# Kernel tuning notes

Hardware: AMD Instinct MI355X
Metric: run time of the kernel (lower is better)

The kernel has to match this reference:

```python
import jax, jax.numpy as jnp
import numpy as np

PROMPT_LEN = 2048
VOCAB = 49408
DIM = 768


def setup_inputs() -> dict:
    key = jax.random.key(0)
    k1, k2 = jax.random.split(key)
    # prompt_embs initialized ~ N(0, 0.02) per nn.init.normal_(std=0.02)
    prompt_embs = jax.random.normal(k1, (PROMPT_LEN, DIM), dtype=jnp.float32) * 0.02
    # codebook (CLIP embedding table), fixed data (not a trainable param)
    clip_embs = jax.random.normal(k2, (VOCAB, DIM), dtype=jnp.float32)
    return {"prompt_embs": prompt_embs, "clip_embs": clip_embs}


def _find_nearest(prompt_embs, clip_embs):
    # torch.cdist with p=2 -> Euclidean distance. argmin is invariant under sqrt,
    # so we use the expanded squared-distance form (single GEMM + norms),
    # avoiding materializing the [P, D]-broadcast difference tensor.
    p_sq = jnp.sum(prompt_embs * prompt_embs, axis=-1, keepdims=True)  # [P, 1]
    c_sq = jnp.sum(clip_embs * clip_embs, axis=-1)                      # [V]
    cross = jnp.einsum("pd,vd->pv", prompt_embs, clip_embs)            # [P, V]
    d2 = p_sq + c_sq[None, :] - 2.0 * cross                             # [P, V]
    return jnp.argmin(d2, axis=1)                                       # [P]


def reference(prompt_embs, clip_embs):
    prompt_ids = _find_nearest(prompt_embs, clip_embs)      # [P] int
    vocab_embs = clip_embs[prompt_ids, :]                   # [P, D] gather
    # straight-through: value = vocab_embs, gradient flows to prompt_embs
    out_embs = jax.lax.stop_gradient(vocab_embs - prompt_embs) + prompt_embs
    return out_embs, prompt_ids
```

## Files before the change

### kernel.cpp

```cpp
#include <hip/hip_runtime.h>
#include <float.h>

#define PROMPT_LEN 2048
#define VOCAB 49408
#define DIM 768
#define ROWS_TOTAL (VOCAB + PROMPT_LEN)
#define NS 8
#define NMI (PROMPT_LEN / 64)
#define BM 64
#define BN 64
#define KCH 128
#define NCHUNK (DIM / KCH)
#define LDK (KCH + 8)
#define CAND_MAX 4096
#define EPS 0.008f

typedef __attribute__((ext_vector_type(8))) short s8v;
typedef __attribute__((ext_vector_type(4))) float fx4;


__device__ inline unsigned short f2bf(float x) {
    unsigned u = __float_as_uint(x);
    u += 0x7FFFu + ((u >> 16) & 1u);
    return (unsigned short)(u >> 16);
}

__device__ inline void merge2(float& b1, float& b2, int& bi,
                              float y1, float y2, int yi) {
    if (y1 < b1) { b2 = fminf(b1, y2); b1 = y1; bi = yi; }
    else         { b2 = fminf(b2, fminf(y1, y2)); }
}

__device__ inline void conv_row(const float* __restrict__ src,
                                unsigned short* __restrict__ dH,
                                unsigned short* __restrict__ dL, int lane) {
    #pragma unroll
    for (int i = 0; i < 3; ++i) {
        float4 x = ((const float4*)src)[i * 64 + lane];
        ushort4 h, l;
        h.x = f2bf(x.x); l.x = f2bf(x.x - __uint_as_float((unsigned)h.x << 16));
        h.y = f2bf(x.y); l.y = f2bf(x.y - __uint_as_float((unsigned)h.y << 16));
        h.z = f2bf(x.z); l.z = f2bf(x.z - __uint_as_float((unsigned)h.z << 16));
        h.w = f2bf(x.w); l.w = f2bf(x.w - __uint_as_float((unsigned)h.w << 16));
        ((ushort4*)dH)[i * 64 + lane] = h;
        ((ushort4*)dL)[i * 64 + lane] = l;
    }
}

__global__ void __launch_bounds__(256) k_sumsq(const float* __restrict__ prompt,
                                               const float* __restrict__ clip,
                                               float* __restrict__ csq,
                                               unsigned* __restrict__ scal) {
    int tid  = threadIdx.x;
    int wid  = tid >> 6;
    int lane = tid & 63;
    int base = blockIdx.x * 32 + wid * 8;

    if (blockIdx.x == 0 && tid == 0) scal[0] = 0u;

    float locMin = FLT_MAX, locMax = 0.f;
    for (int r = base; r < base + 8; r += 2) {
        const float* s0 = (r     < VOCAB) ? clip + (size_t)r * DIM
                                          : prompt + (size_t)(r - VOCAB) * DIM;
        const float* s1 = (r + 1 < VOCAB) ? clip + (size_t)(r + 1) * DIM
                                          : prompt + (size_t)(r + 1 - VOCAB) * DIM;
        float4 a0 = ((const float4*)s0)[lane];
        float4 a1 = ((const float4*)s0)[64 + lane];
        float4 a2 = ((const float4*)s0)[128 + lane];
        float4 b0 = ((const float4*)s1)[lane];
        float4 b1 = ((const float4*)s1)[64 + lane];
        float4 b2 = ((const float4*)s1)[128 + lane];
        float sA = a0.x*a0.x + a0.y*a0.y + a0.z*a0.z + a0.w*a0.w
                 + a1.x*a1.x + a1.y*a1.y + a1.z*a1.z + a1.w*a1.w
                 + a2.x*a2.x + a2.y*a2.y + a2.z*a2.z + a2.w*a2.w;
        float sB = b0.x*b0.x + b0.y*b0.y + b0.z*b0.z + b0.w*b0.w
                 + b1.x*b1.x + b1.y*b1.y + b1.z*b1.z + b1.w*b1.w
                 + b2.x*b2.x + b2.y*b2.y + b2.z*b2.z + b2.w*b2.w;
        #pragma unroll
        for (int m = 32; m >= 1; m >>= 1) {
            sA += __shfl_xor(sA, m, 64);
            sB += __shfl_xor(sB, m, 64);
        }
        if (r < VOCAB)     locMin = fminf(locMin, sA); else locMax = fmaxf(locMax, sA);
        if (r + 1 < VOCAB) locMin = fminf(locMin, sB); else locMax = fmaxf(locMax, sB);
        if (lane == 0) {
            if (r < VOCAB)     csq[r] = sA;
            if (r + 1 < VOCAB) csq[r + 1] = sB;
        }
    }
    __shared__ float smn[4], smx[4];
    if (lane == 0) { smn[wid] = locMin; smx[wid] = locMax; }
    __syncthreads();
    if (tid == 0) {
        float mn = FLT_MAX, mx = 0.f;
        #pragma unroll
        for (int w = 0; w < 4; ++w) { mn = fminf(mn, smn[w]); mx = fmaxf(mx, smx[w]); }
        atomicMin(&scal[1], __float_as_uint(mn));
        atomicMax((int*)&scal[2], (int)__float_as_uint(mx));
    }
}

__global__ void __launch_bounds__(256) k_compact_convert(
        const float* __restrict__ prompt, const float* __restrict__ clip,
        const float* __restrict__ csq,
        int* __restrict__ cand, float* __restrict__ candCsq,
        unsigned* __restrict__ scal, int* __restrict__ cnt,
        unsigned short* __restrict__ PbH, unsigned short* __restrict__ PbL,
        unsigned short* __restrict__ CbH, unsigned short* __restrict__ CbL) {
    float cmin    = __uint_as_float(scal[1]);
    float pmax_sq = __uint_as_float(scal[2]);
    float B  = sqrtf(pmax_sq) * 1.0001f + 1e-6f;
    float U  = cmin + 2.f * B * sqrtf(cmin) + 1.0f;
    float sT = B + sqrtf(B * B + U);
    float T  = sT * sT;

    int tid = threadIdx.x;
    int v   = blockIdx.x * 256 + tid;
    if (blockIdx.x == 0) {
        if (tid == 0) scal[3] = 0u;
        if (tid < NMI) cnt[tid] = 0;
    }
    __shared__ int cntS, basep;
    __shared__ int kvS[256];
    if (tid == 0) cntS = 0;
    __syncthreads();
    float cs = csq[v];
    int keep = (cs <= T);
    int pos = 0;
    if (keep) pos = atomicAdd(&cntS, 1);
    __syncthreads();
    if (tid == 0 && cntS > 0) basep = atomicAdd((int*)&scal[0], cntS);
    __syncthreads();
    if (keep) {
        cand[basep + pos]    = v;
        candCsq[basep + pos] = cs;
        kvS[pos] = v;
    }
    __syncthreads();

    int nk   = cntS;
    int wid  = tid >> 6;
    int lane = tid & 63;
    for (int i = wid; i < nk; i += 4) {
        int dst = basep + i;
        if (dst >= CAND_MAX) break;
        conv_row(clip + (size_t)kvS[i] * DIM,
                 CbH + (size_t)dst * DIM, CbL + (size_t)dst * DIM, lane);
    }
    #pragma unroll
    for (int j = wid; j < 11; j += 4) {
        int r = blockIdx.x + 193 * j;
        if (r < PROMPT_LEN)
            conv_row(prompt + (size_t)r * DIM,
                     PbH + (size_t)r * DIM, PbL + (size_t)r * DIM, lane);
    }
}

__global__ void __launch_bounds__(256, 2)
k_score(const unsigned short* __restrict__ PbH, const unsigned short* __restrict__ PbL,
        const unsigned short* __restrict__ CbH, const unsigned short* __restrict__ CbL,
        const float* __restrict__ candCsq, const int* __restrict__ cand,
        unsigned* __restrict__ scal, int* __restrict__ cnt,
        float* __restrict__ AB1, float* __restrict__ AB2, int* __restrict__ AIdx,
        const float* __restrict__ prompt, const float* __restrict__ clip,
        int* __restrict__ amb, float* __restrict__ out) {
    int mi = blockIdx.x & (NMI - 1);
    int s  = blockIdx.x >> 5;
    int m0 = mi * BM;
    int rawCount = (int)scal[0];
    int count = rawCount > CAND_MAX ? CAND_MAX : rawCount;
    int ntiles = (count + BN - 1) / BN;

    int tid  = threadIdx.x;
    int lane = tid & 63;
    int wid  = tid >> 6;
    int wr32 = (wid >> 1) * 32;
    int wc32 = (wid & 1) * 32;
    int l15  = lane & 15;
    int l4   = lane >> 4;

    __shared__ unsigned short Ah[BM][LDK], Al[BM][LDK];
    __shared__ unsigned short Bh[BN][LDK], Bl[BN][LDK];
    __shared__ int   candS[BN];
    __shared__ float csqS[BN];
    __shared__ float mB1[BM][4], mB2[BM][4];
    __shared__ int   mBI[BM][4];
    __shared__ int   winS[BM], clearS[BM];
    __shared__ int   lastS;

    int srow[4], scol[4], offA[4];
    #pragma unroll
    for (int f = 0; f < 4; ++f) {
        int j = tid + 256 * f;
        srow[f] = j >> 4;
        scol[f] = (j & 15) * 8;
        offA[f] = (m0 + srow[f]) * DIM + scol[f];
    }

    float rb1[2][4], rb2[2][4]; int rbi[2][4];
    #pragma unroll
    for (int fm = 0; fm < 2; ++fm)
        #pragma unroll
        for (int j = 0; j < 4; ++j) { rb1[fm][j] = FLT_MAX; rb2[fm][j] = FLT_MAX; rbi[fm][j] = 0x7fffffff; }

    for (int tile = s; tile < ntiles; tile += NS) {
        __syncthreads();
        if (tid < BN) {
            int ci = tile * BN + tid;
            candS[tid] = (ci < count) ? cand[ci] : 0;
            csqS[tid]  = (ci < count) ? candCsq[ci] : FLT_MAX;
        }

        int offB[4];
        #pragma unroll
        for (int f = 0; f < 4; ++f) {
            int rowc = tile * BN + srow[f];
            if (rowc >= count) rowc = 0;
            offB[f] = rowc * DIM + scol[f];
        }

        fx4 acc00 = {0.f,0.f,0.f,0.f}, acc01 = {0.f,0.f,0.f,0.f};
        fx4 acc10 = {0.f,0.f,0.f,0.f}, acc11 = {0.f,0.f,0.f,0.f};

        s8v rAh[4], rAl[4], rBh[4], rBl[4];
        #pragma unroll
        for (int f = 0; f < 4; ++f) {
            rAh[f] = *(const s8v*)(PbH + offA[f]);
            rAl[f] = *(const s8v*)(PbL + offA[f]);
            rBh[f] = *(const s8v*)(CbH + offB[f]);
            rBl[f] = *(const s8v*)(CbL + offB[f]);
        }

        #pragma unroll
        for (int kc = 0; kc < NCHUNK; ++kc) {
            __syncthreads();
            #pragma unroll
            for (int f = 0; f < 4; ++f) {
                *(s8v*)&Ah[srow[f]][scol[f]] = rAh[f];
                *(s8v*)&Al[srow[f]][scol[f]] = rAl[f];
                *(s8v*)&Bh[srow[f]][scol[f]] = rBh[f];
                *(s8v*)&Bl[srow[f]][scol[f]] = rBl[f];
            }
            __syncthreads();
            if (kc + 1 < NCHUNK) {
                int off = (kc + 1) * KCH;
                #pragma unroll
                for (int f = 0; f < 4; ++f) {
                    rAh[f] = *(const s8v*)(PbH + offA[f] + off);
                    rAl[f] = *(const s8v*)(PbL + offA[f] + off);
                    rBh[f] = *(const s8v*)(CbH + offB[f] + off);
                    rBl[f] = *(const s8v*)(CbL + offB[f] + off);
                }
            }
            #pragma unroll
            for (int kk = 0; kk < KCH / 32; ++kk) {
                int ko = kk * 32 + l4 * 8;
                s8v ah0 = *(const s8v*)&Ah[wr32      + l15][ko];
                s8v ah1 = *(const s8v*)&Ah[wr32 + 16 + l15][ko];
                s8v al0 = *(const s8v*)&Al[wr32      + l15][ko];
                s8v al1 = *(const s8v*)&Al[wr32 + 16 + l15][ko];
                s8v bh0 = *(const s8v*)&Bh[wc32      + l15][ko];
                s8v bh1 = *(const s8v*)&Bh[wc32 + 16 + l15][ko];
                s8v bl0 = *(const s8v*)&Bl[wc32      + l15][ko];
                s8v bl1 = *(const s8v*)&Bl[wc32 + 16 + l15][ko];
                acc00 = __builtin_amdgcn_mfma_f32_16x16x32_bf16(ah0, bh0, acc00, 0, 0, 0);
                acc01 = __builtin_amdgcn_mfma_f32_16x16x32_bf16(ah0, bh1, acc01, 0, 0, 0);
                acc10 = __builtin_amdgcn_mfma_f32_16x16x32_bf16(ah1, bh0, acc10, 0, 0, 0);
                acc11 = __builtin_amdgcn_mfma_f32_16x16x32_bf16(ah1, bh1, acc11, 0, 0, 0);
                acc00 = __builtin_amdgcn_mfma_f32_16x16x32_bf16(al0, bh0, acc00, 0, 0, 0);
                acc01 = __builtin_amdgcn_mfma_f32_16x16x32_bf16(al0, bh1, acc01, 0, 0, 0);
                acc10 = __builtin_amdgcn_mfma_f32_16x16x32_bf16(al1, bh0, acc10, 0, 0, 0);
                acc11 = __builtin_amdgcn_mfma_f32_16x16x32_bf16(al1, bh1, acc11, 0, 0, 0);
                acc00 = __builtin_amdgcn_mfma_f32_16x16x32_bf16(ah0, bl0, acc00, 0, 0, 0);
                acc01 = __builtin_amdgcn_mfma_f32_16x16x32_bf16(ah0, bl1, acc01, 0, 0, 0);
                acc10 = __builtin_amdgcn_mfma_f32_16x16x32_bf16(ah1, bl0, acc10, 0, 0, 0);
                acc11 = __builtin_amdgcn_mfma_f32_16x16x32_bf16(ah1, bl1, acc11, 0, 0, 0);
            }
        }

        float cs0 = csqS[wc32 + l15];       int v0 = candS[wc32 + l15];
        float cs1 = csqS[wc32 + 16 + l15];  int v1 = candS[wc32 + 16 + l15];
        #pragma unroll
        for (int j = 0; j < 4; ++j) {
            if (cs0 < FLT_MAX) {
                float d2 = fmaf(-2.f, acc00[j], cs0);
                if (d2 < rb1[0][j]) { rb2[0][j] = rb1[0][j]; rb1[0][j] = d2; rbi[0][j] = v0; }
                else if (d2 <= rb2[0][j]) rb2[0][j] = d2;
                d2 = fmaf(-2.f, acc10[j], cs0);
                if (d2 < rb1[1][j]) { rb2[1][j] = rb1[1][j]; rb1[1][j] = d2; rbi[1][j] = v0; }
                else if (d2 <= rb2[1][j]) rb2[1][j] = d2;
            }
            if (cs1 < FLT_MAX) {
                float d2 = fmaf(-2.f, acc01[j], cs1);
                if (d2 < rb1[0][j]) { rb2[0][j] = rb1[0][j]; rb1[0][j] = d2; rbi[0][j] = v1; }
                else if (d2 <= rb2[0][j]) rb2[0][j] = d2;
                d2 = fmaf(-2.f, acc11[j], cs1);
                if (d2 < rb1[1][j]) { rb2[1][j] = rb1[1][j]; rb1[1][j] = d2; rbi[1][j] = v1; }
                else if (d2 <= rb2[1][j]) rb2[1][j] = d2;
            }
        }
    }

    #pragma unroll
    for (int fm = 0; fm < 2; ++fm)
        #pragma unroll
        for (int j = 0; j < 4; ++j) {
            float b1 = rb1[fm][j], b2 = rb2[fm][j]; int bi = rbi[fm][j];
            #pragma unroll
            for (int msk = 1; msk <= 8; msk <<= 1) {
                float y1 = __shfl_xor(b1, msk, 64);
                float y2 = __shfl_xor(b2, msk, 64);
                int   yi = __shfl_xor(bi, msk, 64);
                merge2(b1, b2, bi, y1, y2, yi);
            }
            if (l15 == 0) {
                int rl = wr32 + fm * 16 + l4 * 4 + j;
                mB1[rl][wid & 1] = b1; mB2[rl][wid & 1] = b2; mBI[rl][wid & 1] = bi;
            }
        }
    __syncthreads();
    if (tid < BM) {
        float B1 = mB1[tid][0], B2 = mB2[tid][0]; int BI = mBI[tid][0];
        merge2(B1, B2, BI, mB1[tid][1], mB2[tid][1], mBI[tid][1]);
        int m = m0 + tid;
        __hip_atomic_store(&AB1[m * NS + s], B1, __ATOMIC_RELAXED, __HIP_MEMORY_SCOPE_AGENT);
        __hip_atomic_store(&AB2[m * NS + s], B2, __ATOMIC_RELAXED, __HIP_MEMORY_SCOPE_AGENT);
        __hip_atomic_store(&AIdx[m * NS + s], BI, __ATOMIC_RELAXED, __HIP_MEMORY_SCOPE_AGENT);
    }
    __syncthreads();
    if (tid == 0) {
        __threadfence();
        int old = atomicAdd(&cnt[mi], 1);
        lastS = (old == NS - 1);
    }
    __syncthreads();
    if (!lastS) return;
    __threadfence();

    {
        int r = tid & 63, g = tid >> 6;
        int m = m0 + r;
        float b1 = FLT_MAX, b2 = FLT_MAX; int bi = 0x7fffffff;
        #pragma unroll
        for (int ss = 0; ss < 2; ++ss) {
            int s2 = g * 2 + ss;
            float y1 = __hip_atomic_load(&AB1[m * NS + s2], __ATOMIC_RELAXED, __HIP_MEMORY_SCOPE_AGENT);
            float y2 = __hip_atomic_load(&AB2[m * NS + s2], __ATOMIC_RELAXED, __HIP_MEMORY_SCOPE_AGENT);
            int   yi = __hip_atomic_load(&AIdx[m * NS + s2], __ATOMIC_RELAXED, __HIP_MEMORY_SCOPE_AGENT);
            merge2(b1, b2, bi, y1, y2, yi);
        }
        mB1[r][g] = b1; mB2[r][g] = b2; mBI[r][g] = bi;
    }
    __syncthreads();
    if (tid < BM) {
        float B1 = mB1[tid][0], B2 = mB2[tid][0]; int BI = mBI[tid][0];
        #pragma unroll
        for (int gg = 1; gg < 4; ++gg)
            merge2(B1, B2, BI, mB1[tid][gg], mB2[tid][gg], mBI[tid][gg]);
        int clear = (rawCount <= CAND_MAX) && (B2 - B1 >= EPS);
        winS[tid] = BI; clearS[tid] = clear;
        if (!clear) {
            int pos = atomicAdd((int*)&scal[3], 1);
            amb[pos] = m0 + tid;
        }
    }
    __syncthreads();
    for (int rr = wid; rr < BM; rr += 4) {
        if (!clearS[rr]) continue;
        int mm = m0 + rr, win = winS[rr];
        const float* crow = clip + (size_t)win * DIM;
        const float* prow = prompt + (size_t)mm * DIM;
        #pragma unroll
        for (int i = 0; i < 3; ++i) {
            float4 c = ((const float4*)crow)[i * 64 + lane];
            float4 p = ((const float4*)prow)[i * 64 + lane];
            float4 o;
            o.x = (c.x - p.x) + p.x;
            o.y = (c.y - p.y) + p.y;
            o.z = (c.z - p.z) + p.z;
            o.w = (c.w - p.w) + p.w;
            ((float4*)(out + (size_t)mm * DIM))[i * 64 + lane] = o;
        }
        if (lane == 0) out[(size_t)PROMPT_LEN * DIM + mm] = (float)win;
    }
}

__global__ void __launch_bounds__(1024) k_fallback(const float* __restrict__ prompt,
                                                   const float* __restrict__ clip,
                                                   const int* __restrict__ cand,
                                                   const unsigned* __restrict__ scal,
                                                   const int* __restrict__ amb,
                                                   float* __restrict__ out) {
    int nAmb  = (int)scal[3];
    int count = (int)scal[0];
    int tid  = threadIdx.x;
    int wid  = tid >> 6;
    int lane = tid & 63;

    __shared__ double fB[16];
    __shared__ int    fI[16];
    __shared__ int    sWin;

    for (int a = blockIdx.x; a < nAmb; a += gridDim.x) {
        int m = amb[a];
        const float* prow = prompt + (size_t)m * DIM;
        double pd[12];
        #pragma unroll
        for (int i = 0; i < 3; ++i) {
            float4 v = ((const float4*)prow)[i * 64 + lane];
            pd[i*4+0] = (double)v.x; pd[i*4+1] = (double)v.y;
            pd[i*4+2] = (double)v.z; pd[i*4+3] = (double)v.w;
        }
        double best = 1e300;
        int bestIdx = 0x7fffffff;
        for (int ci = wid; ci < count; ci += 16) {
            int v = cand[ci];
            const float* crow = clip + (size_t)v * DIM;
            double sd = 0.0;
            #pragma unroll
            for (int i = 0; i < 3; ++i) {
                float4 c = ((const float4*)crow)[i * 64 + lane];
                double d0 = (double)c.x - pd[i*4+0];
                double d1 = (double)c.y - pd[i*4+1];
                double d2 = (double)c.z - pd[i*4+2];
                double d3 = (double)c.w - pd[i*4+3];
                sd = fma(d0, d0, sd); sd = fma(d1, d1, sd);
                sd = fma(d2, d2, sd); sd = fma(d3, d3, sd);
            }
            #pragma unroll
            for (int msk = 32; msk >= 1; msk >>= 1) sd += __shfl_xor(sd, msk, 64);
            if (sd < best || (sd == best && v < bestIdx)) { best = sd; bestIdx = v; }
        }
        if (lane == 0) { fB[wid] = best; fI[wid] = bestIdx; }
        __syncthreads();
        if (tid == 0) {
            double b = fB[0]; int bi2 = fI[0];
            #pragma unroll
            for (int w = 1; w < 16; ++w)
                if (fB[w] < b || (fB[w] == b && fI[w] < bi2)) { b = fB[w]; bi2 = fI[w]; }
            sWin = bi2;
        }
        __syncthreads();
        int win = sWin;

        if (tid < 192) {
            float4 c = ((const float4*)(clip + (size_t)win * DIM))[tid];
            float4 p = ((const float4*)prow)[tid];
            float4 o;
            o.x = (c.x - p.x) + p.x;
            o.y = (c.y - p.y) + p.y;
            o.z = (c.z - p.z) + p.z;
            o.w = (c.w - p.w) + p.w;
            ((float4*)(out + (size_t)m * DIM))[tid] = o;
        }
        if (tid == 0) out[(size_t)PROMPT_LEN * DIM + m] = (float)win;
        __syncthreads();
    }
}

extern "C" void kernel_launch(void* const* d_in, const int* in_sizes, int n_in,
                              void* d_out, int out_size, void* d_ws, size_t ws_size,
                              hipStream_t stream) {
    const float* prompt = (const float*)d_in[0];
    const float* clip   = (const float*)d_in[1];
    float* out = (float*)d_out;

    char* w = (char*)d_ws;
    float*    csq     = (float*)w;                 w += (size_t)VOCAB * 4;
    int*      cand    = (int*)w;                   w += (size_t)VOCAB * 4;
    float*    candCsq = (float*)w;                 w += (size_t)VOCAB * 4;
    unsigned* scal    = (unsigned*)w;              w += 32;
    float*    AB1     = (float*)w;                 w += (size_t)PROMPT_LEN * NS * 4;
    float*    AB2     = (float*)w;                 w += (size_t)PROMPT_LEN * NS * 4;
    int*      AIdx    = (int*)w;                   w += (size_t)PROMPT_LEN * NS * 4;
    int*      amb     = (int*)w;                   w += (size_t)PROMPT_LEN * 4;
    int*      cnt     = (int*)w;                   w += 128;
    unsigned short* PbH = (unsigned short*)w;      w += (size_t)PROMPT_LEN * DIM * 2;
    unsigned short* PbL = (unsigned short*)w;      w += (size_t)PROMPT_LEN * DIM * 2;
    unsigned short* CbH = (unsigned short*)w;      w += (size_t)CAND_MAX * DIM * 2;
    unsigned short* CbL = (unsigned short*)w;      w += (size_t)CAND_MAX * DIM * 2;

    k_sumsq<<<ROWS_TOTAL / 32, 256, 0, stream>>>(prompt, clip, csq, scal);
    k_compact_convert<<<VOCAB / 256, 256, 0, stream>>>(prompt, clip, csq, cand, candCsq,
                                                       scal, cnt, PbH, PbL, CbH, CbL);
    k_score<<<NMI * NS, 256, 0, stream>>>(PbH, PbL, CbH, CbL, candCsq, cand, scal, cnt,
                                          AB1, AB2, AIdx, prompt, clip, amb, out);
    k_fallback<<<128, 1024, 0, stream>>>(prompt, clip, cand, scal, amb, out);
}
```

Measured before the change: 332.8 us.

## Fuse four kernels into one cooperative persistent kernel with grid syncs

Replaces the four separate launches (sum of squares, compaction/conversion, scoring, fallback) with a single cooperative kernel of 256 blocks. Grid-wide barriers separate the stages. Prompt bf16 hi/lo splitting moves into the sum-of-squares pass so each prompt row is read only once. This removes launch gaps and inter-kernel drains. The costs are that only 256 blocks run the memory-bound stages, the fallback uses 4 waves per block instead of 16, and the grid-sync overhead is added.

```diff
diff --git a/kernel.cpp b/kernel.cpp
--- a/kernel.cpp
+++ b/kernel.cpp
@@ -1,12 +1,15 @@
 #include <hip/hip_runtime.h>
+#include <hip/hip_cooperative_groups.h>
 #include <float.h>
+
+namespace cg = cooperative_groups;
 
 #define PROMPT_LEN 2048
 #define VOCAB 49408
 #define DIM 768
 #define ROWS_TOTAL (VOCAB + PROMPT_LEN)
 #define NS 8
-#define NMI (PROMPT_LEN / 64)
+#define NMI 32
 #define BM 64
 #define BN 64
 #define KCH 128
@@ -25,10 +28,14 @@
     return (unsigned short)(u >> 16);
 }
 
-__device__ inline void merge2(float& b1, float& b2, int& bi,
-                              float y1, float y2, int yi) {
-    if (y1 < b1) { b2 = fminf(b1, y2); b1 = y1; bi = yi; }
-    else         { b2 = fminf(b2, fminf(y1, y2)); }
+__device__ inline void split_store(float4 x, unsigned short* dH, unsigned short* dL, int idx) {
+    ushort4 h, l;
+    h.x = f2bf(x.x); l.x = f2bf(x.x - __uint_as_float((unsigned)h.x << 16));
+    h.y = f2bf(x.y); l.y = f2bf(x.y - __uint_as_float((unsigned)h.y << 16));
+    h.z = f2bf(x.z); l.z = f2bf(x.z - __uint_as_float((unsigned)h.z << 16));
+    h.w = f2bf(x.w); l.w = f2bf(x.w - __uint_as_float((unsigned)h.w << 16));
+    ((ushort4*)dH)[idx] = h;
+    ((ushort4*)dL)[idx] = l;
 }
 
 __device__ inline void conv_row(const float* __restrict__ src,
@@ -37,424 +44,399 @@
     #pragma unroll
     for (int i = 0; i < 3; ++i) {
         float4 x = ((const float4*)src)[i * 64 + lane];
-        ushort4 h, l;
-        h.x = f2bf(x.x); l.x = f2bf(x.x - __uint_as_float((unsigned)h.x << 16));
-        h.y = f2bf(x.y); l.y = f2bf(x.y - __uint_as_float((unsigned)h.y << 16));
-        h.z = f2bf(x.z); l.z = f2bf(x.z - __uint_as_float((unsigned)h.z << 16));
-        h.w = f2bf(x.w); l.w = f2bf(x.w - __uint_as_float((unsigned)h.w << 16));
-        ((ushort4*)dH)[i * 64 + lane] = h;
-        ((ushort4*)dL)[i * 64 + lane] = l;
-    }
-}
-
-__global__ void __launch_bounds__(256) k_sumsq(const float* __restrict__ prompt,
-                                               const float* __restrict__ clip,
-                                               float* __restrict__ csq,
-                                               unsigned* __restrict__ scal) {
+        split_store(x, dH, dL, i * 64 + lane);
+    }
+}
+
+__device__ inline void merge2(float& b1, float& b2, int& bi,
+                              float y1, float y2, int yi) {
+    if (y1 < b1) { b2 = fminf(b1, y2); b1 = y1; bi = yi; }
+    else         { b2 = fminf(b2, fminf(y1, y2)); }
+}
+
+__global__ void __launch_bounds__(256)
+k_all(const float* __restrict__ prompt, const float* __restrict__ clip,
+      float* __restrict__ csq, int* __restrict__ cand, float* __restrict__ candCsq,
+      unsigned* __restrict__ scal,
+      float* __restrict__ AB1, float* __restrict__ AB2, int* __restrict__ AIdx,
+      int* __restrict__ amb,
+      unsigned short* __restrict__ PbH, unsigned short* __restrict__ PbL,
+      unsigned short* __restrict__ CbH, unsigned short* __restrict__ CbL,
+      float* __restrict__ out) {
+    cg::grid_group grid = cg::this_grid();
+
     int tid  = threadIdx.x;
     int wid  = tid >> 6;
     int lane = tid & 63;
-    int base = blockIdx.x * 32 + wid * 8;
-
-    if (blockIdx.x == 0 && tid == 0) scal[0] = 0u;
-
-    float locMin = FLT_MAX, locMax = 0.f;
-    for (int r = base; r < base + 8; r += 2) {
-        const float* s0 = (r     < VOCAB) ? clip + (size_t)r * DIM
-                                          : prompt + (size_t)(r - VOCAB) * DIM;
-        const float* s1 = (r + 1 < VOCAB) ? clip + (size_t)(r + 1) * DIM
-                                          : prompt + (size_t)(r + 1 - VOCAB) * DIM;
-        float4 a0 = ((const float4*)s0)[lane];
-        float4 a1 = ((const float4*)s0)[64 + lane];
-        float4 a2 = ((const float4*)s0)[128 + lane];
-        float4 b0 = ((const float4*)s1)[lane];
-        float4 b1 = ((const float4*)s1)[64 + lane];
-        float4 b2 = ((const float4*)s1)[128 + lane];
-        float sA = a0.x*a0.x + a0.y*a0.y + a0.z*a0.z + a0.w*a0.w
-                 + a1.x*a1.x + a1.y*a1.y + a1.z*a1.z + a1.w*a1.w
-                 + a2.x*a2.x + a2.y*a2.y + a2.z*a2.z + a2.w*a2.w;
-        float sB = b0.x*b0.x + b0.y*b0.y + b0.z*b0.z + b0.w*b0.w
-                 + b1.x*b1.x + b1.y*b1.y + b1.z*b1.z + b1.w*b1.w
-                 + b2.x*b2.x + b2.y*b2.y + b2.z*b2.z + b2.w*b2.w;
-        #pragma unroll
-        for (int m = 32; m >= 1; m >>= 1) {
-            sA += __shfl_xor(sA, m, 64);
-            sB += __shfl_xor(sB, m, 64);
-        }
-        if (r < VOCAB)     locMin = fminf(locMin, sA); else locMax = fmaxf(locMax, sA);
-        if (r + 1 < VOCAB) locMin = fminf(locMin, sB); else locMax = fmaxf(locMax, sB);
-        if (lane == 0) {
-            if (r < VOCAB)     csq[r] = sA;
-            if (r + 1 < VOCAB) csq[r + 1] = sB;
-        }
-    }
-    __shared__ float smn[4], smx[4];
-    if (lane == 0) { smn[wid] = locMin; smx[wid] = locMax; }
-    __syncthreads();
-    if (tid == 0) {
-        float mn = FLT_MAX, mx = 0.f;
-        #pragma unroll
-        for (int w = 0; w < 4; ++w) { mn = fminf(mn, smn[w]); mx = fmaxf(mx, smx[w]); }
-        atomicMin(&scal[1], __float_as_uint(mn));
-        atomicMax((int*)&scal[2], (int)__float_as_uint(mx));
-    }
-}
-
-__global__ void __launch_bounds__(256) k_compact_convert(
-        const float* __restrict__ prompt, const float* __restrict__ clip,
-        const float* __restrict__ csq,
-        int* __restrict__ cand, float* __restrict__ candCsq,
-        unsigned* __restrict__ scal, int* __restrict__ cnt,
-        unsigned short* __restrict__ PbH, unsigned short* __restrict__ PbL,
-        unsigned short* __restrict__ CbH, unsigned short* __restrict__ CbL) {
-    float cmin    = __uint_as_float(scal[1]);
-    float pmax_sq = __uint_as_float(scal[2]);
-    float B  = sqrtf(pmax_sq) * 1.0001f + 1e-6f;
-    float U  = cmin + 2.f * B * sqrtf(cmin) + 1.0f;
-    float sT = B + sqrtf(B * B + U);
-    float T  = sT * sT;
-
-    int tid = threadIdx.x;
-    int v   = blockIdx.x * 256 + tid;
-    if (blockIdx.x == 0) {
-        if (tid == 0) scal[3] = 0u;
-        if (tid < NMI) cnt[tid] = 0;
-    }
-    __shared__ int cntS, basep;
-    __shared__ int kvS[256];
-    if (tid == 0) cntS = 0;
-    __syncthreads();
-    float cs = csq[v];
-    int keep = (cs <= T);
-    int pos = 0;
-    if (keep) pos = atomicAdd(&cntS, 1);
-    __syncthreads();
-    if (tid == 0 && cntS > 0) basep = atomicAdd((int*)&scal[0], cntS);
-    __syncthreads();
-    if (keep) {
-        cand[basep + pos]    = v;
-        candCsq[basep + pos] = cs;
-        kvS[pos] = v;
-    }
-    __syncthreads();
-
-    int nk   = cntS;
-    int wid  = tid >> 6;
-    int lane = tid & 63;
-    for (int i = wid; i < nk; i += 4) {
-        int dst = basep + i;
-        if (dst >= CAND_MAX) break;
-        conv_row(clip + (size_t)kvS[i] * DIM,
-                 CbH + (size_t)dst * DIM, CbL + (size_t)dst * DIM, lane);
-    }
-    #pragma unroll
-    for (int j = wid; j < 11; j += 4) {
-        int r = blockIdx.x + 193 * j;
-        if (r < PROMPT_LEN)
-            conv_row(prompt + (size_t)r * DIM,
-                     PbH + (size_t)r * DIM, PbL + (size_t)r * DIM, lane);
-    }
-}
-
-__global__ void __launch_bounds__(256, 2)
-k_score(const unsigned short* __restrict__ PbH, const unsigned short* __restrict__ PbL,
-        const unsigned short* __restrict__ CbH, const unsigned short* __restrict__ CbL,
-        const float* __restrict__ candCsq, const int* __restrict__ cand,
-        unsigned* __restrict__ scal, int* __restrict__ cnt,
-        float* __restrict__ AB1, float* __restrict__ AB2, int* __restrict__ AIdx,
-        const float* __restrict__ prompt, const float* __restrict__ clip,
-        int* __restrict__ amb, float* __restrict__ out) {
-    int mi = blockIdx.x & (NMI - 1);
-    int s  = blockIdx.x >> 5;
-    int m0 = mi * BM;
-    int rawCount = (int)scal[0];
-    int count = rawCount > CAND_MAX ? CAND_MAX : rawCount;
-    int ntiles = (count + BN - 1) / BN;
-
-    int tid  = threadIdx.x;
-    int lane = tid & 63;
-    int wid  = tid >> 6;
-    int wr32 = (wid >> 1) * 32;
-    int wc32 = (wid & 1) * 32;
-    int l15  = lane & 15;
-    int l4   = lane >> 4;
+    int bx   = blockIdx.x;
 
     __shared__ unsigned short Ah[BM][LDK], Al[BM][LDK];
     __shared__ unsigned short Bh[BN][LDK], Bl[BN][LDK];
     __shared__ int   candS[BN];
     __shared__ float csqS[BN];
-    __shared__ float mB1[BM][4], mB2[BM][4];
-    __shared__ int   mBI[BM][4];
-    __shared__ int   winS[BM], clearS[BM];
-    __shared__ int   lastS;
-
-    int srow[4], scol[4], offA[4];
-    #pragma unroll
-    for (int f = 0; f < 4; ++f) {
-        int j = tid + 256 * f;
-        srow[f] = j >> 4;
-        scol[f] = (j & 15) * 8;
-        offA[f] = (m0 + srow[f]) * DIM + scol[f];
-    }
-
-    float rb1[2][4], rb2[2][4]; int rbi[2][4];
-    #pragma unroll
-    for (int fm = 0; fm < 2; ++fm)
-        #pragma unroll
-        for (int j = 0; j < 4; ++j) { rb1[fm][j] = FLT_MAX; rb2[fm][j] = FLT_MAX; rbi[fm][j] = 0x7fffffff; }
-
-    for (int tile = s; tile < ntiles; tile += NS) {
-        __syncthreads();
-        if (tid < BN) {
-            int ci = tile * BN + tid;
-            candS[tid] = (ci < count) ? cand[ci] : 0;
-            csqS[tid]  = (ci < count) ? candCsq[ci] : FLT_MAX;
-        }
-
-        int offB[4];
+    __shared__ float mB1[BM][2], mB2[BM][2];
+    __shared__ int   mBI[BM][2];
+    __shared__ int   kvS[256];
+    __shared__ int   cntS, basep;
+    __shared__ float smn[4], smx[4];
+    __shared__ double fB[4];
+    __shared__ int    fI[4], sWin;
+
+    if (bx == 0 && tid == 0) { scal[0] = 0u; scal[3] = 0u; }
+    {
+        int gw = bx * 4 + wid;
+        float locMin = FLT_MAX, locMax = 0.f;
+        for (int r0 = gw; r0 < ROWS_TOTAL; r0 += 2048) {
+            int r1 = r0 + 1024;
+            int v1 = (r1 < ROWS_TOTAL);
+            const float* s0 = (r0 < VOCAB) ? clip + (size_t)r0 * DIM
+                                           : prompt + (size_t)(r0 - VOCAB) * DIM;
+            const float* s1 = v1 ? ((r1 < VOCAB) ? clip + (size_t)r1 * DIM
+                                                 : prompt + (size_t)(r1 - VOCAB) * DIM)
+                                 : s0;
+            float4 a0 = ((const float4*)s0)[lane];
+            float4 a1 = ((const float4*)s0)[64 + lane];
+            float4 a2 = ((const float4*)s0)[128 + lane];
+            float4 b0 = ((const float4*)s1)[lane];
+            float4 b1 = ((const float4*)s1)[64 + lane];
+            float4 b2 = ((const float4*)s1)[128 + lane];
+            float sA = a0.x*a0.x + a0.y*a0.y + a0.z*a0.z + a0.w*a0.w
+                     + a1.x*a1.x + a1.y*a1.y + a1.z*a1.z + a1.w*a1.w
+                     + a2.x*a2.x + a2.y*a2.y + a2.z*a2.z + a2.w*a2.w;
+            float sB = b0.x*b0.x + b0.y*b0.y + b0.z*b0.z + b0.w*b0.w
+                     + b1.x*b1.x + b1.y*b1.y + b1.z*b1.z + b1.w*b1.w
+                     + b2.x*b2.x + b2.y*b2.y + b2.z*b2.z + b2.w*b2.w;
+            #pragma unroll
+            for (int m = 32; m >= 1; m >>= 1) {
+                sA += __shfl_xor(sA, m, 64);
+                sB += __shfl_xor(sB, m, 64);
+            }
+            if (r0 < VOCAB) {
+                if (lane == 0) csq[r0] = sA;
+                locMin = fminf(locMin, sA);
+            } else {
+                locMax = fmaxf(locMax, sA);
+                int pr = r0 - VOCAB;
+                unsigned short* dH = PbH + (size_t)pr * DIM;
+                unsigned short* dL = PbL + (size_t)pr * DIM;
+                split_store(a0, dH, dL, lane);
+                split_store(a1, dH, dL, 64 + lane);
+                split_store(a2, dH, dL, 128 + lane);
+            }
+            if (v1) {
+                if (r1 < VOCAB) {
+                    if (lane == 0) csq[r1] = sB;
+                    locMin = fminf(locMin, sB);
+                } else {
+                    locMax = fmaxf(locMax, sB);
+                    int pr = r1 - VOCAB;
+                    unsigned short* dH = PbH + (size_t)pr * DIM;
+                    unsigned short* dL = PbL + (size_t)pr * DIM;
+                    split_store(b0, dH, dL, lane);
+                    split_store(b1, dH, dL, 64 + lane);
+                    split_store(b2, dH, dL, 128 + lane);
+                }
+            }
+        }
+        if (lane == 0) { smn[wid] = locMin; smx[wid] = locMax; }
+        __syncthreads();
+        if (tid == 0) {
+            float mn = FLT_MAX, mx = 0.f;
+            #pragma unroll
+            for (int w = 0; w < 4; ++w) { mn = fminf(mn, smn[w]); mx = fmaxf(mx, smx[w]); }
+            atomicMin(&scal[1], __float_as_uint(mn));
+            atomicMax((int*)&scal[2], (int)__float_as_uint(mx));
+        }
+    }
+    grid.sync();
+
+    {
+        float cmin    = __uint_as_float(scal[1]);
+        float pmax_sq = __uint_as_float(scal[2]);
+        float B  = sqrtf(pmax_sq) * 1.0001f + 1e-6f;
+        float U  = cmin + 2.f * B * sqrtf(cmin) + 1.0f;
+        float sT = B + sqrtf(B * B + U);
+        float T  = sT * sT;
+
+        int v = bx * 256 + tid;
+        if (tid == 0) cntS = 0;
+        __syncthreads();
+        int keep = (v < VOCAB) && (csq[v] <= T);
+        int pos = 0;
+        if (keep) pos = atomicAdd(&cntS, 1);
+        __syncthreads();
+        if (tid == 0 && cntS > 0) basep = atomicAdd((int*)&scal[0], cntS);
+        __syncthreads();
+        if (keep) {
+            int dst = basep + pos;
+            cand[dst]    = v;
+            candCsq[dst] = csq[v];
+            kvS[pos] = v;
+        }
+        __syncthreads();
+        int nk = cntS;
+        for (int i = wid; i < nk; i += 4) {
+            int dst = basep + i;
+            if (dst >= CAND_MAX) break;
+            conv_row(clip + (size_t)kvS[i] * DIM,
+                     CbH + (size_t)dst * DIM, CbL + (size_t)dst * DIM, lane);
+        }
+    }
+    grid.sync();
+
+    int rawCount = (int)scal[0];
+    int count = rawCount > CAND_MAX ? CAND_MAX : rawCount;
+
+    {
+        int mi = bx & (NMI - 1);
+        int s  = bx >> 5;
+        int m0 = mi * BM;
+        int ntiles = (count + BN - 1) / BN;
+
+        int wr32 = (wid >> 1) * 32;
+        int wc32 = (wid & 1) * 32;
+        int l15  = lane & 15;
+        int l4   = lane >> 4;
+
+        int srow[4], scol[4], offA[4];
         #pragma unroll
         for (int f = 0; f < 4; ++f) {
-            int rowc = tile * BN + srow[f];
-            if (rowc >= count) rowc = 0;
-            offB[f] = rowc * DIM + scol[f];
-        }
-
-        fx4 acc00 = {0.f,0.f,0.f,0.f}, acc01 = {0.f,0.f,0.f,0.f};
-        fx4 acc10 = {0.f,0.f,0.f,0.f}, acc11 = {0.f,0.f,0.f,0.f};
-
-        s8v rAh[4], rAl[4], rBh[4], rBl[4];
+            int j = tid + 256 * f;
+            srow[f] = j >> 4;
+            scol[f] = (j & 15) * 8;
+            offA[f] = (m0 + srow[f]) * DIM + scol[f];
+        }
+
+        float rb1[2][4], rb2[2][4]; int rbi[2][4];
         #pragma unroll
-        for (int f = 0; f < 4; ++f) {
-            rAh[f] = *(const s8v*)(PbH + offA[f]);
-            rAl[f] = *(const s8v*)(PbL + offA[f]);
-            rBh[f] = *(const s8v*)(CbH + offB[f]);
-            rBl[f] = *(const s8v*)(CbL + offB[f]);
-        }
-
+        for (int fm = 0; fm < 2; ++fm)
+            #pragma unroll
+            for (int j = 0; j < 4; ++j) { rb1[fm][j] = FLT_MAX; rb2[fm][j] = FLT_MAX; rbi[fm][j] = 0x7fffffff; }
+
+        for (int tile = s; tile < ntiles; tile += NS) {
+            __syncthreads();
+            if (tid < BN) {
+                int ci = tile * BN + tid;
+                candS[tid] = (ci < count) ? cand[ci] : 0;
+                csqS[tid]  = (ci < count) ? candCsq[ci] : FLT_MAX;
+            }
+
+            int offB[4];
+            #pragma unroll
+            for (int f = 0; f < 4; ++f) {
+                int rowc = tile * BN + srow[f];
+                if (rowc >= count) rowc = 0;
+                offB[f] = rowc * DIM + scol[f];
+            }
+
+            fx4 acc00 = {0.f,0.f,0.f,0.f}, acc01 = {0.f,0.f,0.f,0.f};
+            fx4 acc10 = {0.f,0.f,0.f,0.f}, acc11 = {0.f,0.f,0.f,0.f};
+
+            s8v rAh[4], rAl[4], rBh[4], rBl[4];
+            #pragma unroll
+            for (int f = 0; f < 4; ++f) {
+                rAh[f] = *(const s8v*)(PbH + offA[f]);
+                rAl[f] = *(const s8v*)(PbL + offA[f]);
+                rBh[f] = *(const s8v*)(CbH + offB[f]);
+                rBl[f] = *(const s8v*)(CbL + offB[f]);
+            }
+
+            #pragma unroll
+            for (int kc = 0; kc < NCHUNK; ++kc) {
+                __syncthreads();
+                #pragma unroll
+                for (int f = 0; f < 4; ++f) {
+                    *(s8v*)&Ah[srow[f]][scol[f]] = rAh[f];
+                    *(s8v*)&Al[srow[f]][scol[f]] = rAl[f];
+                    *(s8v*)&Bh[srow[f]][scol[f]] = rBh[f];
+                    *(s8v*)&Bl[srow[f]][scol[f]] = rBl[f];
+                }
+                __syncthreads();
+                if (kc + 1 < NCHUNK) {
+                    int off = (kc + 1) * KCH;
+                    #pragma unroll
+                    for (int f = 0; f < 4; ++f) {
+                        rAh[f] = *(const s8v*)(PbH + offA[f] + off);
+                        rAl[f] = *(const s8v*)(PbL + offA[f] + off);
+                        rBh[f] = *(const s8v*)(CbH + offB[f] + off);
+                        rBl[f] = *(const s8v*)(CbL + offB[f] + off);
+                    }
+                }
+                #pragma unroll
+                for (int kk = 0; kk < KCH / 32; ++kk) {
+                    int ko = kk * 32 + l4 * 8;
+                    s8v ah0 = *(const s8v*)&Ah[wr32      + l15][ko];
+                    s8v ah1 = *(const s8v*)&Ah[wr32 + 16 + l15][ko];
+                    s8v al0 = *(const s8v*)&Al[wr32      + l15][ko];
+                    s8v al1 = *(const s8v*)&Al[wr32 + 16 + l15][ko];
+                    s8v bh0 = *(const s8v*)&Bh[wc32      + l15][ko];
+                    s8v bh1 = *(const s8v*)&Bh[wc32 + 16 + l15][ko];
+                    s8v bl0 = *(const s8v*)&Bl[wc32      + l15][ko];
+                    s8v bl1 = *(const s8v*)&Bl[wc32 + 16 + l15][ko];
+                    acc00 = __builtin_amdgcn_mfma_f32_16x16x32_bf16(ah0, bh0, acc00, 0, 0, 0);
+                    acc01 = __builtin_amdgcn_mfma_f32_16x16x32_bf16(ah0, bh1, acc01, 0, 0, 0);
+                    acc10 = __builtin_amdgcn_mfma_f32_16x16x32_bf16(ah1, bh0, acc10, 0, 0, 0);
+                    acc11 = __builtin_amdgcn_mfma_f32_16x16x32_bf16(ah1, bh1, acc11, 0, 0, 0);
+                    acc00 = __builtin_amdgcn_mfma_f32_16x16x32_bf16(al0, bh0, acc00, 0, 0, 0);
+                    acc01 = __builtin_amdgcn_mfma_f32_16x16x32_bf16(al0, bh1, acc01, 0, 0, 0);
+                    acc10 = __builtin_amdgcn_mfma_f32_16x16x32_bf16(al1, bh0, acc10, 0, 0, 0);
+                    acc11 = __builtin_amdgcn_mfma_f32_16x16x32_bf16(al1, bh1, acc11, 0, 0, 0);
+                    acc00 = __builtin_amdgcn_mfma_f32_16x16x32_bf16(ah0, bl0, acc00, 0, 0, 0);
+                    acc01 = __builtin_amdgcn_mfma_f32_16x16x32_bf16(ah0, bl1, acc01, 0, 0, 0);
+                    acc10 = __builtin_amdgcn_mfma_f32_16x16x32_bf16(ah1, bl0, acc10, 0, 0, 0);
+                    acc11 = __builtin_amdgcn_mfma_f32_16x16x32_bf16(ah1, bl1, acc11, 0, 0, 0);
+                }
+            }
+
+            float cs0 = csqS[wc32 + l15];       int v0 = candS[wc32 + l15];
+            float cs1 = csqS[wc32 + 16 + l15];  int v1 = candS[wc32 + 16 + l15];
+            #pragma unroll
+            for (int j = 0; j < 4; ++j) {
+                if (cs0 < FLT_MAX) {
+                    float d2 = fmaf(-2.f, acc00[j], cs0);
+                    if (d2 < rb1[0][j]) { rb2[0][j] = rb1[0][j]; rb1[0][j] = d2; rbi[0][j] = v0; }
+                    else if (d2 <= rb2[0][j]) rb2[0][j] = d2;
+                    d2 = fmaf(-2.f, acc10[j], cs0);
+                    if (d2 < rb1[1][j]) { rb2[1][j] = rb1[1][j]; rb1[1][j] = d2; rbi[1][j] = v0; }
+                    else if (d2 <= rb2[1][j]) rb2[1][j] = d2;
+                }
+                if (cs1 < FLT_MAX) {
+                    float d2 = fmaf(-2.f, acc01[j], cs1);
+                    if (d2 < rb1[0][j]) { rb2[0][j] = rb1[0][j]; rb1[0][j] = d2; rbi[0][j] = v1; }
+                    else if (d2 <= rb2[0][j]) rb2[0][j] = d2;
+                    d2 = fmaf(-2.f, acc11[j], cs1);
+                    if (d2 < rb1[1][j]) { rb2[1][j] = rb1[1][j]; rb1[1][j] = d2; rbi[1][j] = v1; }
+                    else if (d2 <= rb2[1][j]) rb2[1][j] = d2;
+                }
+            }
+        }
+
+        __syncthreads();
         #pragma unroll
-        for (int kc = 0; kc < NCHUNK; ++kc) {
-            __syncthreads();
-            #pragma unroll
-            for (int f = 0; f < 4; ++f) {
-                *(s8v*)&Ah[srow[f]][scol[f]] = rAh[f];
-                *(s8v*)&Al[srow[f]][scol[f]] = rAl[f];
-                *(s8v*)&Bh[srow[f]][scol[f]] = rBh[f];
-                *(s8v*)&Bl[srow[f]][scol[f]] = rBl[f];
-            }
-            __syncthreads();
-            if (kc + 1 < NCHUNK) {
-                int off = (kc + 1) * KCH;
-                #pragma unroll
-                for (int f = 0; f < 4; ++f) {
-                    rAh[f] = *(const s8v*)(PbH + offA[f] + off);
-                    rAl[f] = *(const s8v*)(PbL + offA[f] + off);
-                    rBh[f] = *(const s8v*)(CbH + offB[f] + off);
-                    rBl[f] = *(const s8v*)(CbL + offB[f] + off);
-                }
-            }
-            #pragma unroll
-            for (int kk = 0; kk < KCH / 32; ++kk) {
-                int ko = kk * 32 + l4 * 8;
-                s8v ah0 = *(const s8v*)&Ah[wr32      + l15][ko];
-                s8v ah1 = *(const s8v*)&Ah[wr32 + 16 + l15][ko];
-                s8v al0 = *(const s8v*)&Al[wr32      + l15][ko];
-                s8v al1 = *(const s8v*)&Al[wr32 + 16 + l15][ko];
-                s8v bh0 = *(const s8v*)&Bh[wc32      + l15][ko];
-                s8v bh1 = *(const s8v*)&Bh[wc32 + 16 + l15][ko];
-                s8v bl0 = *(const s8v*)&Bl[wc32      + l15][ko];
-                s8v bl1 = *(const s8v*)&Bl[wc32 + 16 + l15][ko];
-                acc00 = __builtin_amdgcn_mfma_f32_16x16x32_bf16(ah0, bh0, acc00, 0, 0, 0);
-                acc01 = __builtin_amdgcn_mfma_f32_16x16x32_bf16(ah0, bh1, acc01, 0, 0, 0);
-                acc10 = __builtin_amdgcn_mfma_f32_16x16x32_bf16(ah1, bh0, acc10, 0, 0, 0);
-                acc11 = __builtin_amdgcn_mfma_f32_16x16x32_bf16(ah1, bh1, acc11, 0, 0, 0);
-                acc00 = __builtin_amdgcn_mfma_f32_16x16x32_bf16(al0, bh0, acc00, 0, 0, 0);
-                acc01 = __builtin_amdgcn_mfma_f32_16x16x32_bf16(al0, bh1, acc01, 0, 0, 0);
-                acc10 = __builtin_amdgcn_mfma_f32_16x16x32_bf16(al1, bh0, acc10, 0, 0, 0);
-                acc11 = __builtin_amdgcn_mfma_f32_16x16x32_bf16(al1, bh1, acc11, 0, 0, 0);
-                acc00 = __builtin_amdgcn_mfma_f32_16x16x32_bf16(ah0, bl0, acc00, 0, 0, 0);
-                acc01 = __builtin_amdgcn_mfma_f32_16x16x32_bf16(ah0, bl1, acc01, 0, 0, 0);
-                acc10 = __builtin_amdgcn_mfma_f32_16x16x32_bf16(ah1, bl0, acc10, 0, 0, 0);
-                acc11 = __builtin_amdgcn_mfma_f32_16x16x32_bf16(ah1, bl1, acc11, 0, 0, 0);
-            }
-        }
-
-        float cs0 = csqS[wc32 + l15];       int v0 = candS[wc32 + l15];
-        float cs1 = csqS[wc32 + 16 + l15];  int v1 = candS[wc32 + 16 + l15];
-        #pragma unroll
-        for (int j = 0; j < 4; ++j) {
-            if (cs0 < FLT_MAX) {
-                float d2 = fmaf(-2.f, acc00[j], cs0);
-                if (d2 < rb1[0][j]) { rb2[0][j] = rb1[0][j]; rb1[0][j] = d2; rbi[0][j] = v0; }
-                else if (d2 <= rb2[0][j]) rb2[0][j] = d2;
-                d2 = fmaf(-2.f, acc10[j], cs0);
-                if (d2 < rb1[1][j]) { rb2[1][j] = rb1[1][j]; rb1[1][j] = d2; rbi[1][j] = v0; }
-                else if (d2 <= rb2[1][j]) rb2[1][j] = d2;
-            }
-            if (cs1 < FLT_MAX) {
-                float d2 = fmaf(-2.f, acc01[j], cs1);
-                if (d2 < rb1[0][j]) { rb2[0][j] = rb1[0][j]; rb1[0][j] = d2; rbi[0][j] = v1; }
-                else if (d2 <= rb2[0][j]) rb2[0][j] = d2;
-                d2 = fmaf(-2.f, acc11[j], cs1);
-                if (d2 < rb1[1][j]) { rb2[1][j] = rb1[1][j]; rb1[1][j] = d2; rbi[1][j] = v1; }
-                else if (d2 <= rb2[1][j]) rb2[1][j] = d2;
-            }
-        }
-    }
-
-    #pragma unroll
-    for (int fm = 0; fm < 2; ++fm)
-        #pragma unroll
-        for (int j = 0; j < 4; ++j) {
-            float b1 = rb1[fm][j], b2 = rb2[fm][j]; int bi = rbi[fm][j];
-            #pragma unroll
-            for (int msk = 1; msk <= 8; msk <<= 1) {
+        for (int fm = 0; fm < 2; ++fm)
+            #pragma unroll
+            for (int j = 0; j < 4; ++j) {
+                float b1 = rb1[fm][j], b2 = rb2[fm][j]; int bi = rbi[fm][j];
+                #pragma unroll
+                for (int msk = 1; msk <= 8; msk <<= 1) {
+                    float y1 = __shfl_xor(b1, msk, 64);
+                    float y2 = __shfl_xor(b2, msk, 64);
+                    int   yi = __shfl_xor(bi, msk, 64);
+                    merge2(b1, b2, bi, y1, y2, yi);
+                }
+                if (l15 == 0) {
+                    int rl = wr32 + fm * 16 + l4 * 4 + j;
+                    mB1[rl][wid & 1] = b1; mB2[rl][wid & 1] = b2; mBI[rl][wid & 1] = bi;
+                }
+            }
+        __syncthreads();
+        if (tid < BM) {
+            float B1 = mB1[tid][0], B2 = mB2[tid][0]; int BI = mBI[tid][0];
+            merge2(B1, B2, BI, mB1[tid][1], mB2[tid][1], mBI[tid][1]);
+            int m = m0 + tid;
+            AB1[m * NS + s]  = B1;
+            AB2[m * NS + s]  = B2;
+            AIdx[m * NS + s] = BI;
+        }
+    }
+    grid.sync();
+
+    {
+        int gw = bx * 4 + wid;
+        for (int m = gw; m < PROMPT_LEN; m += 1024) {
+            int s = lane & 7;
+            float b1 = AB1[m * NS + s];
+            float b2 = AB2[m * NS + s];
+            int   bi = AIdx[m * NS + s];
+            #pragma unroll
+            for (int msk = 1; msk <= 4; msk <<= 1) {
                 float y1 = __shfl_xor(b1, msk, 64);
                 float y2 = __shfl_xor(b2, msk, 64);
                 int   yi = __shfl_xor(bi, msk, 64);
                 merge2(b1, b2, bi, y1, y2, yi);
             }
-            if (l15 == 0) {
-                int rl = wr32 + fm * 16 + l4 * 4 + j;
-                mB1[rl][wid & 1] = b1; mB2[rl][wid & 1] = b2; mBI[rl][wid & 1] = bi;
-            }
-        }
-    __syncthreads();
-    if (tid < BM) {
-        float B1 = mB1[tid][0], B2 = mB2[tid][0]; int BI = mBI[tid][0];
-        merge2(B1, B2, BI, mB1[tid][1], mB2[tid][1], mBI[tid][1]);
-        int m = m0 + tid;
-        __hip_atomic_store(&AB1[m * NS + s], B1, __ATOMIC_RELAXED, __HIP_MEMORY_SCOPE_AGENT);
-        __hip_atomic_store(&AB2[m * NS + s], B2, __ATOMIC_RELAXED, __HIP_MEMORY_SCOPE_AGENT);
-        __hip_atomic_store(&AIdx[m * NS + s], BI, __ATOMIC_RELAXED, __HIP_MEMORY_SCOPE_AGENT);
-    }
-    __syncthreads();
-    if (tid == 0) {
-        __threadfence();
-        int old = atomicAdd(&cnt[mi], 1);
-        lastS = (old == NS - 1);
-    }
-    __syncthreads();
-    if (!lastS) return;
-    __threadfence();
+            if (rawCount > CAND_MAX || b2 - b1 < EPS) {
+                if (lane == 0) {
+                    int pos = atomicAdd((int*)&scal[3], 1);
+                    amb[pos] = m;
+                }
+            } else {
+                const float* crow = clip + (size_t)bi * DIM;
+                const float* prow = prompt + (size_t)m * DIM;
+                #pragma unroll
+                for (int i = 0; i < 3; ++i) {
+                    float4 c = ((const float4*)crow)[i * 64 + lane];
+                    float4 p = ((const float4*)prow)[i * 64 + lane];
+                    float4 o;
+                    o.x = (c.x - p.x) + p.x;
+                    o.y = (c.y - p.y) + p.y;
+                    o.z = (c.z - p.z) + p.z;
+                    o.w = (c.w - p.w) + p.w;
+                    ((float4*)(out + (size_t)m * DIM))[i * 64 + lane] = o;
+                }
+                if (lane == 0) out[(size_t)PROMPT_LEN * DIM + m] = (float)bi;
+            }
+        }
+    }
+    grid.sync();
 
     {
-        int r = tid & 63, g = tid >> 6;
-        int m = m0 + r;
-        float b1 = FLT_MAX, b2 = FLT_MAX; int bi = 0x7fffffff;
-        #pragma unroll
-        for (int ss = 0; ss < 2; ++ss) {
-            int s2 = g * 2 + ss;
-            float y1 = __hip_atomic_load(&AB1[m * NS + s2], __ATOMIC_RELAXED, __HIP_MEMORY_SCOPE_AGENT);
-            float y2 = __hip_atomic_load(&AB2[m * NS + s2], __ATOMIC_RELAXED, __HIP_MEMORY_SCOPE_AGENT);
-            int   yi = __hip_atomic_load(&AIdx[m * NS + s2], __ATOMIC_RELAXED, __HIP_MEMORY_SCOPE_AGENT);
-            merge2(b1, b2, bi, y1, y2, yi);
-        }
-        mB1[r][g] = b1; mB2[r][g] = b2; mBI[r][g] = bi;
-    }
-    __syncthreads();
-    if (tid < BM) {
-        float B1 = mB1[tid][0], B2 = mB2[tid][0]; int BI = mBI[tid][0];
-        #pragma unroll
-        for (int gg = 1; gg < 4; ++gg)
-            merge2(B1, B2, BI, mB1[tid][gg], mB2[tid][gg], mBI[tid][gg]);
-        int clear = (rawCount <= CAND_MAX) && (B2 - B1 >= EPS);
-        winS[tid] = BI; clearS[tid] = clear;
-        if (!clear) {
-            int pos = atomicAdd((int*)&scal[3], 1);
-            amb[pos] = m0 + tid;
-        }
-    }
-    __syncthreads();
-    for (int rr = wid; rr < BM; rr += 4) {
-        if (!clearS[rr]) continue;
-        int mm = m0 + rr, win = winS[rr];
-        const float* crow = clip + (size_t)win * DIM;
-        const float* prow = prompt + (size_t)mm * DIM;
-        #pragma unroll
-        for (int i = 0; i < 3; ++i) {
-            float4 c = ((const float4*)crow)[i * 64 + lane];
-            float4 p = ((const float4*)prow)[i * 64 + lane];
-            float4 o;
-            o.x = (c.x - p.x) + p.x;
-            o.y = (c.y - p.y) + p.y;
-            o.z = (c.z - p.z) + p.z;
-            o.w = (c.w - p.w) + p.w;
-            ((float4*)(out + (size_t)mm * DIM))[i * 64 + lane] = o;
-        }
-        if (lane == 0) out[(size_t)PROMPT_LEN * DIM + mm] = (float)win;
-    }
-}
-
-__global__ void __launch_bounds__(1024) k_fallback(const float* __restrict__ prompt,
-                                                   const float* __restrict__ clip,
-                                                   const int* __restrict__ cand,
-                                                   const unsigned* __restrict__ scal,
-                                                   const int* __restrict__ amb,
-                                                   float* __restrict__ out) {
-    int nAmb  = (int)scal[3];
-    int count = (int)scal[0];
-    int tid  = threadIdx.x;
-    int wid  = tid >> 6;
-    int lane = tid & 63;
-
-    __shared__ double fB[16];
-    __shared__ int    fI[16];
-    __shared__ int    sWin;
-
-    for (int a = blockIdx.x; a < nAmb; a += gridDim.x) {
-        int m = amb[a];
-        const float* prow = prompt + (size_t)m * DIM;
-        double pd[12];
-        #pragma unroll
-        for (int i = 0; i < 3; ++i) {
-            float4 v = ((const float4*)prow)[i * 64 + lane];
-            pd[i*4+0] = (double)v.x; pd[i*4+1] = (double)v.y;
-            pd[i*4+2] = (double)v.z; pd[i*4+3] = (double)v.w;
-        }
-        double best = 1e300;
-        int bestIdx = 0x7fffffff;
-        for (int ci = wid; ci < count; ci += 16) {
-            int v = cand[ci];
-            const float* crow = clip + (size_t)v * DIM;
-            double sd = 0.0;
+        int nAmb = (int)scal[3];
+        for (int a = bx; a < nAmb; a += 256) {
+            int m = amb[a];
+            const float* prow = prompt + (size_t)m * DIM;
+            double pd[12];
             #pragma unroll
             for (int i = 0; i < 3; ++i) {
-                float4 c = ((const float4*)crow)[i * 64 + lane];
-                double d0 = (double)c.x - pd[i*4+0];
-                double d1 = (double)c.y - pd[i*4+1];
-                double d2 = (double)c.z - pd[i*4+2];
-                double d3 = (double)c.w - pd[i*4+3];
-                sd = fma(d0, d0, sd); sd = fma(d1, d1, sd);
-                sd = fma(d2, d2, sd); sd = fma(d3, d3, sd);
-            }
-            #pragma unroll
-            for (int msk = 32; msk >= 1; msk >>= 1) sd += __shfl_xor(sd, msk, 64);
-            if (sd < best || (sd == best && v < bestIdx)) { best = sd; bestIdx = v; }
-        }
-        if (lane == 0) { fB[wid] = best; fI[wid] = bestIdx; }
-        __syncthreads();
-        if (tid == 0) {
-            double b = fB[0]; int bi2 = fI[0];
-            #pragma unroll
-            for (int w = 1; w < 16; ++w)
-                if (fB[w] < b || (fB[w] == b && fI[w] < bi2)) { b = fB[w]; bi2 = fI[w]; }
-            sWin = bi2;
-        }
-        __syncthreads();
-        int win = sWin;
-
-        if (tid < 192) {
-            float4 c = ((const float4*)(clip + (size_t)win * DIM))[tid];
-            float4 p = ((const float4*)prow)[tid];
-            float4 o;
-            o.x = (c.x - p.x) + p.x;
-            o.y = (c.y - p.y) + p.y;
-            o.z = (c.z - p.z) + p.z;
-            o.w = (c.w - p.w) + p.w;
-            ((float4*)(out + (size_t)m * DIM))[tid] = o;
-        }
-        if (tid == 0) out[(size_t)PROMPT_LEN * DIM + m] = (float)win;
-        __syncthreads();
+                float4 v = ((const float4*)prow)[i * 64 + lane];
+                pd[i*4+0] = (double)v.x; pd[i*4+1] = (double)v.y;
+                pd[i*4+2] = (double)v.z; pd[i*4+3] = (double)v.w;
+            }
+            double best = 1e300;
+            int bestIdx = 0x7fffffff;
+            for (int ci = wid; ci < rawCount; ci += 4) {
+                int v = cand[ci];
+                const float* crow = clip + (size_t)v * DIM;
+                double sd = 0.0;
+                #pragma unroll
+                for (int i = 0; i < 3; ++i) {
+                    float4 c = ((const float4*)crow)[i * 64 + lane];
+                    double d0 = (double)c.x - pd[i*4+0];
+                    double d1 = (double)c.y - pd[i*4+1];
+                    double d2 = (double)c.z - pd[i*4+2];
+                    double d3 = (double)c.w - pd[i*4+3];
+                    sd = fma(d0, d0, sd); sd = fma(d1, d1, sd);
+                    sd = fma(d2, d2, sd); sd = fma(d3, d3, sd);
+                }
+                #pragma unroll
+                for (int msk = 32; msk >= 1; msk >>= 1) sd += __shfl_xor(sd, msk, 64);
+                if (sd < best || (sd == best && v < bestIdx)) { best = sd; bestIdx = v; }
+            }
+            if (lane == 0) { fB[wid] = best; fI[wid] = bestIdx; }
+            __syncthreads();
+            if (tid == 0) {
+                double b = fB[0]; int bi2 = fI[0];
+                #pragma unroll
+                for (int w = 1; w < 4; ++w)
+                    if (fB[w] < b || (fB[w] == b && fI[w] < bi2)) { b = fB[w]; bi2 = fI[w]; }
+                sWin = bi2;
+            }
+            __syncthreads();
+            int win = sWin;
+
+            if (tid < 192) {
+                float4 c = ((const float4*)(clip + (size_t)win * DIM))[tid];
+                float4 p = ((const float4*)prow)[tid];
+                float4 o;
+                o.x = (c.x - p.x) + p.x;
+                o.y = (c.y - p.y) + p.y;
+                o.z = (c.z - p.z) + p.z;
+                o.w = (c.w - p.w) + p.w;
+                ((float4*)(out + (size_t)m * DIM))[tid] = o;
+            }
+            if (tid == 0) out[(size_t)PROMPT_LEN * DIM + m] = (float)win;
+            __syncthreads();
+        }
     }
 }
 
@@ -474,16 +456,16 @@
     float*    AB2     = (float*)w;                 w += (size_t)PROMPT_LEN * NS * 4;
     int*      AIdx    = (int*)w;                   w += (size_t)PROMPT_LEN * NS * 4;
     int*      amb     = (int*)w;                   w += (size_t)PROMPT_LEN * 4;
-    int*      cnt     = (int*)w;                   w += 128;
     unsigned short* PbH = (unsigned short*)w;      w += (size_t)PROMPT_LEN * DIM * 2;
     unsigned short* PbL = (unsigned short*)w;      w += (size_t)PROMPT_LEN * DIM * 2;
     unsigned short* CbH = (unsigned short*)w;      w += (size_t)CAND_MAX * DIM * 2;
     unsigned short* CbL = (unsigned short*)w;      w += (size_t)CAND_MAX * DIM * 2;
 
-    k_sumsq<<<ROWS_TOTAL / 32, 256, 0, stream>>>(prompt, clip, csq, scal);
-    k_compact_convert<<<VOCAB / 256, 256, 0, stream>>>(prompt, clip, csq, cand, candCsq,
-                                                       scal, cnt, PbH, PbL, CbH, CbL);
-    k_score<<<NMI * NS, 256, 0, stream>>>(PbH, PbL, CbH, CbL, candCsq, cand, scal, cnt,
-                                          AB1, AB2, AIdx, prompt, clip, amb, out);
-    k_fallback<<<128, 1024, 0, stream>>>(prompt, clip, cand, scal, amb, out);
-}
+    void* args[] = {
+        (void*)&prompt, (void*)&clip, (void*)&csq, (void*)&cand, (void*)&candCsq,
+        (void*)&scal, (void*)&AB1, (void*)&AB2, (void*)&AIdx, (void*)&amb,
+        (void*)&PbH, (void*)&PbL, (void*)&CbH, (void*)&CbL, (void*)&out
+    };
+    hipLaunchCooperativeKernel((const void*)k_all, dim3(256), dim3(256),
+                               args, 0, stream);
+}
```

New measurement: 504.1 us. 51.5% more time.
